# Kernel optimization log

Hardware: AMD Instinct MI355X
Metric: run time of the kernel (lower is better)

The kernel has to match this reference:

```python
import jax, jax.numpy as jnp
import numpy as np

N = 100_000      # nodes
E = 1_250_000    # edges (avg degree ~12.5)
D_IN, D_H, D_OUT = 64, 64, 64


def setup_inputs() -> dict:
    key = jax.random.key(0)
    ks = jax.random.split(key, 7)
    x = jax.random.normal(ks[0], (N, D_IN), dtype=jnp.float32)
    edge_index = jax.random.randint(ks[1], (2, E), 0, N, dtype=jnp.int32)
    edge_weight = jax.random.uniform(ks[2], (E,), dtype=jnp.float32)
    # GCNConv linear weights: PyG lin stores [out, in], applied as x @ W.T; bias added after aggregation.
    W1 = jax.random.normal(ks[3], (D_H, D_IN), dtype=jnp.float32) * (1.0 / np.sqrt(D_IN))
    b1 = jax.random.normal(ks[4], (D_H,), dtype=jnp.float32) * 0.01
    W2 = jax.random.normal(ks[5], (D_OUT, D_H), dtype=jnp.float32) * (1.0 / np.sqrt(D_H))
    b2 = jax.random.normal(ks[6], (D_OUT,), dtype=jnp.float32) * 0.01
    return {"x": x, "edge_index": edge_index, "edge_weight": edge_weight,
            "W1": W1, "b1": b1, "W2": W2, "b2": b2}


def _gcn_conv(x, src, dst, w, W, b, n_nodes):
    # PyG GCNConv: add self-loops (weight 1), symmetric normalization, linear, scatter-add, +bias.
    deg = jax.ops.segment_sum(w, dst, num_segments=n_nodes) + 1.0  # +1 from self-loop
    dis = jnp.where(deg > 0, jax.lax.rsqrt(deg), 0.0)              # deg^{-1/2}
    coef = dis[src] * w * dis[dst]                                 # per-edge norm, [E]
    h = x @ W.T                                                    # [N, out]
    agg = jax.ops.segment_sum(h[src] * coef[:, None], dst, num_segments=n_nodes)
    agg = agg + h * (dis * dis)[:, None]                           # self-loop: dis_i * 1 * dis_i
    return agg + b


def reference(x, edge_index, edge_weight, W1, b1, W2, b2):
    n = x.shape[0]
    src, dst = edge_index[0], edge_index[1]
    h = _gcn_conv(x, src, dst, edge_weight, W1, b1, n)
    h = jax.nn.relu(h)
    # dropout p=0.0 -> identity
    return _gcn_conv(h, src, dst, edge_weight, W2, b2, n)
```

## Files before the change

### kernel.cpp

```cpp
#include <hip/hip_runtime.h>


typedef unsigned int u32;
typedef unsigned short u16;

#define NBKT 256
#define LSH 9
#define BNODES 512
#define CAP 8192
#define SRCBITS 17
#define SRCMASK ((1u << SRCBITS) - 1u)

__device__ inline u16 f2bf(float f) {
  u32 u = __float_as_uint(f);
  u32 r = u + 0x7FFFu + ((u >> 16) & 1u);
  return (u16)(r >> 16);
}
__device__ inline float bf_lo(u32 p) { return __uint_as_float(p << 16); }
__device__ inline float bf_hi(u32 p) { return __uint_as_float(p & 0xFFFF0000u); }

__device__ inline u32 blockscan256_excl(u32 val, u32* wsum) {
  int lane = threadIdx.x & 63, wv = threadIdx.x >> 6;
  u32 inc = val;
  #pragma unroll
  for (int d = 1; d < 64; d <<= 1) {
    u32 t = __shfl_up(inc, d);
    if (lane >= d) inc += t;
  }
  if (lane == 63) wsum[wv] = inc;
  __syncthreads();
  u32 off = 0;
  #pragma unroll
  for (int i = 0; i < 4; ++i) if (i < wv) off += wsum[i];
  return off + inc - val;
}

__global__ void k_bin(const int* __restrict__ ei, u32* __restrict__ bucket_cnt,
                      u32* __restrict__ blockbase, int E, int chunk) {
  __shared__ u32 hist[NBKT];
  if (threadIdx.x < NBKT) hist[threadIdx.x] = 0u;
  __syncthreads();
  int e0 = blockIdx.x * chunk;
  int e1 = min(E, e0 + chunk);
  for (int e = e0 + (threadIdx.x << 1); e < e1; e += 512) {
    if (e + 1 < e1) {
      int2 dd = *(const int2*)(ei + E + e);
      atomicAdd(&hist[dd.x >> LSH], 1u);
      atomicAdd(&hist[dd.y >> LSH], 1u);
    } else {
      atomicAdd(&hist[ei[E + e] >> LSH], 1u);
    }
  }
  __syncthreads();
  if (threadIdx.x < NBKT)
    blockbase[threadIdx.x * 256 + blockIdx.x] =
        atomicAdd(&bucket_cnt[threadIdx.x], hist[threadIdx.x]);
}

__global__ __launch_bounds__(256, 4) void k_scatter_gemm(
    const int* __restrict__ ei, const float* __restrict__ w,
    const u32* __restrict__ blockbase,
    uint2* __restrict__ bucketed,
    const float* __restrict__ X, const float* __restrict__ W,
    u16* __restrict__ H, int N, int E, int chunk) {
  __shared__ float Wt[64 * 65];
  __shared__ float Xs[16 * 64];
  __shared__ u32 base[NBKT];
  int tid = threadIdx.x;
  if ((int)blockIdx.x < 256) {
    if (tid < NBKT)
      base[tid] = (u32)tid * CAP + blockbase[tid * 256 + blockIdx.x];
    __syncthreads();
    int e0 = blockIdx.x * chunk, e1 = min(E, e0 + chunk);
    for (int e = e0 + (tid << 1); e < e1; e += 512) {
      if (e + 1 < e1) {
        int2 ss = *(const int2*)(ei + e);
        int2 dd = *(const int2*)(ei + E + e);
        float2 wv = *(const float2*)(w + e);
        u32 p0 = atomicAdd(&base[dd.x >> LSH], 1u);
        u32 p1 = atomicAdd(&base[dd.y >> LSH], 1u);
        bucketed[p0] = make_uint2((u32)ss.x | ((u32)(dd.x & (BNODES - 1)) << SRCBITS),
                                  __float_as_uint(wv.x));
        bucketed[p1] = make_uint2((u32)ss.y | ((u32)(dd.y & (BNODES - 1)) << SRCBITS),
                                  __float_as_uint(wv.y));
      } else {
        int s = ei[e], d = ei[E + e];
        u32 pos = atomicAdd(&base[d >> LSH], 1u);
        bucketed[pos] = make_uint2((u32)s | ((u32)(d & (BNODES - 1)) << SRCBITS),
                                   __float_as_uint(w[e]));
      }
    }
    return;
  }
  int row0 = ((int)blockIdx.x - 256) * 16;
  if (row0 >= N) return;
  for (int i = tid; i < 4096; i += 256) Wt[(i & 63) * 65 + (i >> 6)] = W[i];
  {
    const float4* xsrc = (const float4*)(X + (size_t)row0 * 64);
    if (row0 + 16 <= N) {
      ((float4*)Xs)[tid] = xsrc[tid];
    } else {
      int r = tid >> 4;
      ((float4*)Xs)[tid] = (row0 + r < N) ? xsrc[tid]
                                          : make_float4(0.f, 0.f, 0.f, 0.f);
    }
  }
  __syncthreads();
  int lane = tid & 63, wv4 = tid >> 6;
  int rbase = wv4 * 4;
  float a0 = 0.f, a1 = 0.f, a2 = 0.f, a3 = 0.f;
  #pragma unroll 4
  for (int k4 = 0; k4 < 16; ++k4) {
    int k = k4 << 2;
    float w0 = Wt[k * 65 + lane], w1 = Wt[(k + 1) * 65 + lane];
    float w2 = Wt[(k + 2) * 65 + lane], w3 = Wt[(k + 3) * 65 + lane];
    float4 xa = *(const float4*)&Xs[(rbase + 0) * 64 + k];
    float4 xb = *(const float4*)&Xs[(rbase + 1) * 64 + k];
    float4 xc = *(const float4*)&Xs[(rbase + 2) * 64 + k];
    float4 xd = *(const float4*)&Xs[(rbase + 3) * 64 + k];
    a0 = fmaf(xa.x, w0, fmaf(xa.y, w1, fmaf(xa.z, w2, fmaf(xa.w, w3, a0))));
    a1 = fmaf(xb.x, w0, fmaf(xb.y, w1, fmaf(xb.z, w2, fmaf(xb.w, w3, a1))));
    a2 = fmaf(xc.x, w0, fmaf(xc.y, w1, fmaf(xc.z, w2, fmaf(xc.w, w3, a2))));
    a3 = fmaf(xd.x, w0, fmaf(xd.y, w1, fmaf(xd.z, w2, fmaf(xd.w, w3, a3))));
  }
  int row = row0 + rbase;
  if (row + 3 < N) {
    H[(size_t)row * 64 + lane]       = f2bf(a0);
    H[(size_t)(row + 1) * 64 + lane] = f2bf(a1);
    H[(size_t)(row + 2) * 64 + lane] = f2bf(a2);
    H[(size_t)(row + 3) * 64 + lane] = f2bf(a3);
  } else {
    if (row < N)     H[(size_t)row * 64 + lane]       = f2bf(a0);
    if (row + 1 < N) H[(size_t)(row + 1) * 64 + lane] = f2bf(a1);
    if (row + 2 < N) H[(size_t)(row + 2) * 64 + lane] = f2bf(a2);
    if (row + 3 < N) H[(size_t)(row + 3) * 64 + lane] = f2bf(a3);
  }
}

__global__ void k_statsfill(const uint2* __restrict__ bucketed,
                            const u32* __restrict__ bucket_cnt,
                            float* __restrict__ dis, int4* __restrict__ info,
                            int2* __restrict__ csr, u16* __restrict__ H, int N) {
  __shared__ u32 hist[BNODES];
  __shared__ u32 cur[BNODES];
  __shared__ float disl[BNODES];
  __shared__ u32 wsum[4];
  int b = blockIdx.x, tid = threadIdx.x;
  for (int i = tid; i < BNODES; i += 256) hist[i] = 0u;
  __syncthreads();
  u32 s0 = (u32)b * CAP, s1 = s0 + bucket_cnt[b];
  for (u32 p = s0 + tid; p < s1; p += 256) {
    uint2 ed = bucketed[p];
    u32 local = ed.x >> SRCBITS;
    u32 wfix = (u32)(__uint_as_float(ed.y) * 262144.0f);
    atomicAdd(&hist[local], (1u << 24) | wfix);
  }
  __syncthreads();
  u32 h0 = hist[2 * tid], h1 = hist[2 * tid + 1];
  u32 c0 = h0 >> 24, c1 = h1 >> 24;
  u32 excl = blockscan256_excl(c0 + c1, wsum);
  float d0 = rsqrtf(1.0f + (float)(h0 & 0xFFFFFFu) * (1.0f / 262144.0f));
  float d1 = rsqrtf(1.0f + (float)(h1 & 0xFFFFFFu) * (1.0f / 262144.0f));
  cur[2 * tid] = excl;
  cur[2 * tid + 1] = excl + c0;
  disl[2 * tid] = d0;
  disl[2 * tid + 1] = d1;
  int n0 = b * BNODES + 2 * tid;
  if (n0 < N) {
    dis[n0] = d0;
    info[n0] = make_int4((int)(s0 + excl), (int)c0, __float_as_int(d0), 0);
  }
  if (n0 + 1 < N) {
    dis[n0 + 1] = d1;
    info[n0 + 1] = make_int4((int)(s0 + excl + c0), (int)c1, __float_as_int(d1), 0);
  }
  __syncthreads();
  for (u32 p = s0 + tid; p < s1; p += 256) {
    uint2 ed = bucketed[p];
    u32 local = ed.x >> SRCBITS;
    u32 pos = atomicAdd(&cur[local], 1u);
    csr[s0 + pos] = make_int2((int)(ed.x & SRCMASK), (int)ed.y);
  }
  uint2* Hv = (uint2*)H;
  for (int i = tid; i < BNODES * 16; i += 256) {
    int row = i >> 4;
    int node = b * BNODES + row;
    if (node >= N) break;
    float dv = disl[row];
    size_t idx = (size_t)node * 16 + (i & 15);
    uint2 v = Hv[idx];
    u32 lo = (u32)f2bf(bf_lo(v.x) * dv) | ((u32)f2bf(bf_hi(v.x) * dv) << 16);
    u32 hi = (u32)f2bf(bf_lo(v.y) * dv) | ((u32)f2bf(bf_hi(v.y) * dv) << 16);
    Hv[idx] = make_uint2(lo, hi);
  }
}

__global__ __launch_bounds__(256, 6) void k_agg_gemm(
    const u16* __restrict__ H, const int4* __restrict__ info,
    const int2* __restrict__ csr, const float* __restrict__ bias,
    const float* __restrict__ W2, const float* __restrict__ dis,
    u16* __restrict__ H2, int N) {
  __shared__ float Wt[64 * 65];
  __shared__ float Ys[16 * 64];
  int tid = threadIdx.x;
  for (int i = tid; i < 4096; i += 256) Wt[(i & 63) * 65 + (i >> 6)] = W2[i];
  int node = blockIdx.x * 16 + (tid >> 4);
  int fid = (tid & 15) << 2;
  bool valid = node < N;
  int4 nfo = valid ? info[node] : make_int4(0, 0, 0, 0);
  int s0 = nfo.x, n = nfo.y;
  float d = __int_as_float(nfo.z);
  uint2 hs = valid ? *(const uint2*)(H + (size_t)node * 64 + fid)
                   : make_uint2(0u, 0u);
  float4 b4 = *(const float4*)(bias + fid);
  float4 acc = make_float4(0.f, 0.f, 0.f, 0.f);
  int nm1 = n - 1;
  for (int base = 0; base < n; base += 4) {
    int q1 = min(base + 1, nm1);
    int q2 = min(base + 2, nm1), q3 = min(base + 3, nm1);
    int2 c0 = csr[s0 + base];
    int2 c1 = csr[s0 + q1];
    int2 c2 = csr[s0 + q2];
    int2 c3 = csr[s0 + q3];
    uint2 h0 = *(const uint2*)(H + (size_t)c0.x * 64 + fid);
    uint2 h1 = *(const uint2*)(H + (size_t)c1.x * 64 + fid);
    uint2 h2 = *(const uint2*)(H + (size_t)c2.x * 64 + fid);
    uint2 h3 = *(const uint2*)(H + (size_t)c3.x * 64 + fid);
    float f0 = __int_as_float(c0.y);
    float f1 = (base + 1 < n) ? __int_as_float(c1.y) : 0.f;
    float f2 = (base + 2 < n) ? __int_as_float(c2.y) : 0.f;
    float f3 = (base + 3 < n) ? __int_as_float(c3.y) : 0.f;
    acc.x = fmaf(bf_lo(h0.x), f0, acc.x); acc.y = fmaf(bf_hi(h0.x), f0, acc.y);
    acc.z = fmaf(bf_lo(h0.y), f0, acc.z); acc.w = fmaf(bf_hi(h0.y), f0, acc.w);
    acc.x = fmaf(bf_lo(h1.x), f1, acc.x); acc.y = fmaf(bf_hi(h1.x), f1, acc.y);
    acc.z = fmaf(bf_lo(h1.y), f1, acc.z); acc.w = fmaf(bf_hi(h1.y), f1, acc.w);
    acc.x = fmaf(bf_lo(h2.x), f2, acc.x); acc.y = fmaf(bf_hi(h2.x), f2, acc.y);
    acc.z = fmaf(bf_lo(h2.y), f2, acc.z); acc.w = fmaf(bf_hi(h2.y), f2, acc.w);
    acc.x = fmaf(bf_lo(h3.x), f3, acc.x); acc.y = fmaf(bf_hi(h3.x), f3, acc.y);
    acc.z = fmaf(bf_lo(h3.y), f3, acc.z); acc.w = fmaf(bf_hi(h3.y), f3, acc.w);
  }
  if (valid) {
    acc.x = fmaxf((acc.x + bf_lo(hs.x)) * d + b4.x, 0.f);
    acc.y = fmaxf((acc.y + bf_hi(hs.x)) * d + b4.y, 0.f);
    acc.z = fmaxf((acc.z + bf_lo(hs.y)) * d + b4.z, 0.f);
    acc.w = fmaxf((acc.w + bf_hi(hs.y)) * d + b4.w, 0.f);
  } else {
    acc = make_float4(0.f, 0.f, 0.f, 0.f);
  }
  *(float4*)&Ys[(tid >> 4) * 64 + fid] = acc;
  __syncthreads();
  int lane = tid & 63, wv = tid >> 6;
  int rbase = wv * 4;
  int row0 = blockIdx.x * 16;
  float a0 = 0.f, a1 = 0.f, a2 = 0.f, a3 = 0.f;
  #pragma unroll 4
  for (int k4 = 0; k4 < 16; ++k4) {
    int k = k4 << 2;
    float w0 = Wt[k * 65 + lane], w1 = Wt[(k + 1) * 65 + lane];
    float w2 = Wt[(k + 2) * 65 + lane], w3 = Wt[(k + 3) * 65 + lane];
    float4 xa = *(const float4*)&Ys[(rbase + 0) * 64 + k];
    float4 xb = *(const float4*)&Ys[(rbase + 1) * 64 + k];
    float4 xc = *(const float4*)&Ys[(rbase + 2) * 64 + k];
    float4 xd = *(const float4*)&Ys[(rbase + 3) * 64 + k];
    a0 = fmaf(xa.x, w0, fmaf(xa.y, w1, fmaf(xa.z, w2, fmaf(xa.w, w3, a0))));
    a1 = fmaf(xb.x, w0, fmaf(xb.y, w1, fmaf(xb.z, w2, fmaf(xb.w, w3, a1))));
    a2 = fmaf(xc.x, w0, fmaf(xc.y, w1, fmaf(xc.z, w2, fmaf(xc.w, w3, a2))));
    a3 = fmaf(xd.x, w0, fmaf(xd.y, w1, fmaf(xd.z, w2, fmaf(xd.w, w3, a3))));
  }
  int row = row0 + rbase;
  if (row + 3 < N) {
    float dv0 = dis[row], dv1 = dis[row + 1], dv2 = dis[row + 2], dv3 = dis[row + 3];
    H2[(size_t)row * 64 + lane]       = f2bf(a0 * dv0);
    H2[(size_t)(row + 1) * 64 + lane] = f2bf(a1 * dv1);
    H2[(size_t)(row + 2) * 64 + lane] = f2bf(a2 * dv2);
    H2[(size_t)(row + 3) * 64 + lane] = f2bf(a3 * dv3);
  } else {
    if (row < N)     H2[(size_t)row * 64 + lane]       = f2bf(a0 * dis[row]);
    if (row + 1 < N) H2[(size_t)(row + 1) * 64 + lane] = f2bf(a1 * dis[row + 1]);
    if (row + 2 < N) H2[(size_t)(row + 2) * 64 + lane] = f2bf(a2 * dis[row + 2]);
    if (row + 3 < N) H2[(size_t)(row + 3) * 64 + lane] = f2bf(a3 * dis[row + 3]);
  }
}

__global__ __launch_bounds__(256, 8) void k_aggregate2(
    const u16* __restrict__ H, const int4* __restrict__ info,
    const int2* __restrict__ csr, const float* __restrict__ bias,
    float* __restrict__ Y, int N) {
  int tid = threadIdx.x;
  int node = blockIdx.x * 16 + (tid >> 4);
  int fid = (tid & 15) << 2;
  bool valid = node < N;
  int4 nfo = valid ? info[node] : make_int4(0, 0, 0, 0);
  int s0 = nfo.x, n = nfo.y;
  float d = __int_as_float(nfo.z);
  uint2 hs = valid ? *(const uint2*)(H + (size_t)node * 64 + fid)
                   : make_uint2(0u, 0u);
  float4 b4 = *(const float4*)(bias + fid);
  float4 acc = make_float4(0.f, 0.f, 0.f, 0.f);
  int nm1 = n - 1;
  for (int base = 0; base < n; base += 4) {
    int q1 = min(base + 1, nm1);
    int q2 = min(base + 2, nm1), q3 = min(base + 3, nm1);
    int2 c0 = csr[s0 + base];
    int2 c1 = csr[s0 + q1];
    int2 c2 = csr[s0 + q2];
    int2 c3 = csr[s0 + q3];
    uint2 h0 = *(const uint2*)(H + (size_t)c0.x * 64 + fid);
    uint2 h1 = *(const uint2*)(H + (size_t)c1.x * 64 + fid);
    uint2 h2 = *(const uint2*)(H + (size_t)c2.x * 64 + fid);
    uint2 h3 = *(const uint2*)(H + (size_t)c3.x * 64 + fid);
    float f0 = __int_as_float(c0.y);
    float f1 = (base + 1 < n) ? __int_as_float(c1.y) : 0.f;
    float f2 = (base + 2 < n) ? __int_as_float(c2.y) : 0.f;
    float f3 = (base + 3 < n) ? __int_as_float(c3.y) : 0.f;
    acc.x = fmaf(bf_lo(h0.x), f0, acc.x); acc.y = fmaf(bf_hi(h0.x), f0, acc.y);
    acc.z = fmaf(bf_lo(h0.y), f0, acc.z); acc.w = fmaf(bf_hi(h0.y), f0, acc.w);
    acc.x = fmaf(bf_lo(h1.x), f1, acc.x); acc.y = fmaf(bf_hi(h1.x), f1, acc.y);
    acc.z = fmaf(bf_lo(h1.y), f1, acc.z); acc.w = fmaf(bf_hi(h1.y), f1, acc.w);
    acc.x = fmaf(bf_lo(h2.x), f2, acc.x); acc.y = fmaf(bf_hi(h2.x), f2, acc.y);
    acc.z = fmaf(bf_lo(h2.y), f2, acc.z); acc.w = fmaf(bf_hi(h2.y), f2, acc.w);
    acc.x = fmaf(bf_lo(h3.x), f3, acc.x); acc.y = fmaf(bf_hi(h3.x), f3, acc.y);
    acc.z = fmaf(bf_lo(h3.y), f3, acc.z); acc.w = fmaf(bf_hi(h3.y), f3, acc.w);
  }
  if (valid) {
    acc.x = (acc.x + bf_lo(hs.x)) * d + b4.x;
    acc.y = (acc.y + bf_hi(hs.x)) * d + b4.y;
    acc.z = (acc.z + bf_lo(hs.y)) * d + b4.z;
    acc.w = (acc.w + bf_hi(hs.y)) * d + b4.w;
    *(float4*)(Y + (size_t)node * 64 + fid) = acc;
  }
}

extern "C" void kernel_launch(void* const* d_in, const int* in_sizes, int n_in,
                              void* d_out, int out_size, void* d_ws, size_t ws_size,
                              hipStream_t stream) {
  const float* x  = (const float*)d_in[0];
  const int*   ei = (const int*)d_in[1];
  const float* w  = (const float*)d_in[2];
  const float* W1 = (const float*)d_in[3];
  const float* b1 = (const float*)d_in[4];
  const float* W2 = (const float*)d_in[5];
  const float* b2 = (const float*)d_in[6];
  const int N = in_sizes[0] / 64;
  const int E = in_sizes[2];

  char* ws = (char*)d_ws;
  size_t off = 0;
  auto alloc = [&](size_t bytes) -> char* {
    char* p = ws + off;
    off = (off + bytes + 255) & ~(size_t)255;
    return p;
  };
  u32*   bucket_cnt   = (u32*)  alloc((size_t)NBKT * 4);
  u32*   blockbase    = (u32*)  alloc((size_t)NBKT * 256 * 4);
  uint2* bucketed     = (uint2*)alloc((size_t)NBKT * CAP * 8);
  int2*  csr          = (int2*) alloc((size_t)NBKT * CAP * 8);
  float* dis          = (float*)alloc((size_t)N * 4);
  int4*  info         = (int4*) alloc((size_t)N * 16);
  u16*   h1           = (u16*)  alloc((size_t)N * 64 * 2);
  u16*   h2           = (u16*)  alloc((size_t)N * 64 * 2);

  const int chunk = ((E + 511) / 512) * 2;
  const int nbG = (N + 15) / 16;
  const int nbA = (N + 15) / 16;
  const int nbB = (N + BNODES - 1) >> LSH;

  hipMemsetAsync(bucket_cnt, 0, (size_t)NBKT * 4, stream);
  k_bin<<<256, 256, 0, stream>>>(ei, bucket_cnt, blockbase, E, chunk);
  k_scatter_gemm<<<256 + nbG, 256, 0, stream>>>(ei, w, blockbase, bucketed,
                                                x, W1, h1, N, E, chunk);
  k_statsfill<<<nbB, 256, 0, stream>>>(bucketed, bucket_cnt, dis, info, csr, h1, N);
  k_agg_gemm<<<nbA, 256, 0, stream>>>(h1, info, csr, b1, W2, dis, h2, N);
  k_aggregate2<<<nbA, 256, 0, stream>>>(h2, info, csr, b2, (float*)d_out, N);
}
```

Baseline: 237.3 us.

## Pad CSR rows to multiples of four and degree-sort nodes within buckets

Each node's CSR segment is padded to a multiple of four with zero-weight entries, so the aggregation loops read two aligned int4 pairs per step with no clamping or masking. k_statsfill also builds a per-bucket permutation that orders nodes by in-degree (capped at 63) using a 64-bin counting sort. The aggregation kernels then process nodes in that order, so the 16-thread groups in a wavefront see similar loop trip counts and diverge less. The cost is extra CSR storage (CAP raised to 9216), an indirection through perm, scattered output writes, and padded entries that still gather row 0 of H.

```diff
diff --git a/kernel.cpp b/kernel.cpp
--- a/kernel.cpp
+++ b/kernel.cpp
@@ -7,7 +7,7 @@
 #define NBKT 256
 #define LSH 9
 #define BNODES 512
-#define CAP 8192
+#define CAP 9216
 #define SRCBITS 17
 #define SRCMASK ((1u << SRCBITS) - 1u)
 
@@ -140,13 +140,17 @@
 __global__ void k_statsfill(const uint2* __restrict__ bucketed,
                             const u32* __restrict__ bucket_cnt,
                             float* __restrict__ dis, int4* __restrict__ info,
-                            int2* __restrict__ csr, u16* __restrict__ H, int N) {
+                            int2* __restrict__ csr, u32* __restrict__ perm,
+                            u16* __restrict__ H, int N) {
   __shared__ u32 hist[BNODES];
   __shared__ u32 cur[BNODES];
   __shared__ float disl[BNODES];
   __shared__ u32 wsum[4];
+  __shared__ u32 dbin[64];
+  __shared__ u32 drank[64];
   int b = blockIdx.x, tid = threadIdx.x;
   for (int i = tid; i < BNODES; i += 256) hist[i] = 0u;
+  if (tid < 64) dbin[tid] = 0u;
   __syncthreads();
   u32 s0 = (u32)b * CAP, s1 = s0 + bucket_cnt[b];
   for (u32 p = s0 + tid; p < s1; p += 256) {
@@ -158,23 +162,41 @@
   __syncthreads();
   u32 h0 = hist[2 * tid], h1 = hist[2 * tid + 1];
   u32 c0 = h0 >> 24, c1 = h1 >> 24;
-  u32 excl = blockscan256_excl(c0 + c1, wsum);
+  u32 p0 = (c0 + 3u) & ~3u, p1 = (c1 + 3u) & ~3u;
+  u32 excl = blockscan256_excl(p0 + p1, wsum);
   float d0 = rsqrtf(1.0f + (float)(h0 & 0xFFFFFFu) * (1.0f / 262144.0f));
   float d1 = rsqrtf(1.0f + (float)(h1 & 0xFFFFFFu) * (1.0f / 262144.0f));
   cur[2 * tid] = excl;
-  cur[2 * tid + 1] = excl + c0;
+  cur[2 * tid + 1] = excl + p0;
   disl[2 * tid] = d0;
   disl[2 * tid + 1] = d1;
   int n0 = b * BNODES + 2 * tid;
-  if (n0 < N) {
+  bool v0 = n0 < N, v1 = n0 + 1 < N;
+  if (v0) {
     dis[n0] = d0;
-    info[n0] = make_int4((int)(s0 + excl), (int)c0, __float_as_int(d0), 0);
-  }
-  if (n0 + 1 < N) {
+    info[n0] = make_int4((int)(s0 + excl), (int)p0, __float_as_int(d0), 0);
+    atomicAdd(&dbin[min(c0, 63u)], 1u);
+  }
+  if (v1) {
     dis[n0 + 1] = d1;
-    info[n0 + 1] = make_int4((int)(s0 + excl + c0), (int)c1, __float_as_int(d1), 0);
-  }
-  __syncthreads();
+    info[n0 + 1] = make_int4((int)(s0 + excl + p0), (int)p1, __float_as_int(d1), 0);
+    atomicAdd(&dbin[min(c1, 63u)], 1u);
+  }
+  __syncthreads();
+  if (tid < 64) {
+    u32 v = dbin[tid], inc = v;
+    #pragma unroll
+    for (int d = 1; d < 64; d <<= 1) {
+      u32 t = __shfl_up(inc, d);
+      if (tid >= d) inc += t;
+    }
+    drank[tid] = inc - v;
+  }
+  __syncthreads();
+  if (v0) { u32 r = atomicAdd(&drank[min(c0, 63u)], 1u); perm[b * BNODES + r] = (u32)n0; }
+  if (v1) { u32 r = atomicAdd(&drank[min(c1, 63u)], 1u); perm[b * BNODES + r] = (u32)(n0 + 1); }
+  for (u32 j = c0; j < p0; ++j) csr[s0 + excl + j] = make_int2(0, 0);
+  for (u32 j = c1; j < p1; ++j) csr[s0 + excl + p0 + j] = make_int2(0, 0);
   for (u32 p = s0 + tid; p < s1; p += 256) {
     uint2 ed = bucketed[p];
     u32 local = ed.x >> SRCBITS;
@@ -197,39 +219,36 @@
 
 __global__ __launch_bounds__(256, 6) void k_agg_gemm(
     const u16* __restrict__ H, const int4* __restrict__ info,
-    const int2* __restrict__ csr, const float* __restrict__ bias,
-    const float* __restrict__ W2, const float* __restrict__ dis,
-    u16* __restrict__ H2, int N) {
+    const int2* __restrict__ csr, const u32* __restrict__ perm,
+    const float* __restrict__ bias, const float* __restrict__ W2,
+    const float* __restrict__ dis, u16* __restrict__ H2, int N) {
   __shared__ float Wt[64 * 65];
   __shared__ float Ys[16 * 64];
+  __shared__ u32 nids[16];
   int tid = threadIdx.x;
   for (int i = tid; i < 4096; i += 256) Wt[(i & 63) * 65 + (i >> 6)] = W2[i];
-  int node = blockIdx.x * 16 + (tid >> 4);
+  int slot = blockIdx.x * 16 + (tid >> 4);
   int fid = (tid & 15) << 2;
-  bool valid = node < N;
-  int4 nfo = valid ? info[node] : make_int4(0, 0, 0, 0);
+  bool valid = slot < N;
+  int nid = valid ? (int)perm[slot] : 0;
+  int4 nfo = valid ? info[nid] : make_int4(0, 0, 0, 0);
   int s0 = nfo.x, n = nfo.y;
   float d = __int_as_float(nfo.z);
-  uint2 hs = valid ? *(const uint2*)(H + (size_t)node * 64 + fid)
+  uint2 hs = valid ? *(const uint2*)(H + (size_t)nid * 64 + fid)
                    : make_uint2(0u, 0u);
   float4 b4 = *(const float4*)(bias + fid);
+  if ((tid & 15) == 0) nids[tid >> 4] = valid ? (u32)nid : 0xFFFFFFFFu;
   float4 acc = make_float4(0.f, 0.f, 0.f, 0.f);
-  int nm1 = n - 1;
+  const int4* c4 = (const int4*)(csr + s0);
   for (int base = 0; base < n; base += 4) {
-    int q1 = min(base + 1, nm1);
-    int q2 = min(base + 2, nm1), q3 = min(base + 3, nm1);
-    int2 c0 = csr[s0 + base];
-    int2 c1 = csr[s0 + q1];
-    int2 c2 = csr[s0 + q2];
-    int2 c3 = csr[s0 + q3];
-    uint2 h0 = *(const uint2*)(H + (size_t)c0.x * 64 + fid);
-    uint2 h1 = *(const uint2*)(H + (size_t)c1.x * 64 + fid);
-    uint2 h2 = *(const uint2*)(H + (size_t)c2.x * 64 + fid);
-    uint2 h3 = *(const uint2*)(H + (size_t)c3.x * 64 + fid);
-    float f0 = __int_as_float(c0.y);
-    float f1 = (base + 1 < n) ? __int_as_float(c1.y) : 0.f;
-    float f2 = (base + 2 < n) ? __int_as_float(c2.y) : 0.f;
-    float f3 = (base + 3 < n) ? __int_as_float(c3.y) : 0.f;
+    int4 ca = c4[base >> 1];
+    int4 cb = c4[(base >> 1) + 1];
+    uint2 h0 = *(const uint2*)(H + (size_t)ca.x * 64 + fid);
+    uint2 h1 = *(const uint2*)(H + (size_t)ca.z * 64 + fid);
+    uint2 h2 = *(const uint2*)(H + (size_t)cb.x * 64 + fid);
+    uint2 h3 = *(const uint2*)(H + (size_t)cb.z * 64 + fid);
+    float f0 = __int_as_float(ca.y), f1 = __int_as_float(ca.w);
+    float f2 = __int_as_float(cb.y), f3 = __int_as_float(cb.w);
     acc.x = fmaf(bf_lo(h0.x), f0, acc.x); acc.y = fmaf(bf_hi(h0.x), f0, acc.y);
     acc.z = fmaf(bf_lo(h0.y), f0, acc.z); acc.w = fmaf(bf_hi(h0.y), f0, acc.w);
     acc.x = fmaf(bf_lo(h1.x), f1, acc.x); acc.y = fmaf(bf_hi(h1.x), f1, acc.y);
@@ -251,7 +270,6 @@
   __syncthreads();
   int lane = tid & 63, wv = tid >> 6;
   int rbase = wv * 4;
-  int row0 = blockIdx.x * 16;
   float a0 = 0.f, a1 = 0.f, a2 = 0.f, a3 = 0.f;
   #pragma unroll 4
   for (int k4 = 0; k4 < 16; ++k4) {
@@ -267,52 +285,40 @@
     a2 = fmaf(xc.x, w0, fmaf(xc.y, w1, fmaf(xc.z, w2, fmaf(xc.w, w3, a2))));
     a3 = fmaf(xd.x, w0, fmaf(xd.y, w1, fmaf(xd.z, w2, fmaf(xd.w, w3, a3))));
   }
-  int row = row0 + rbase;
-  if (row + 3 < N) {
-    float dv0 = dis[row], dv1 = dis[row + 1], dv2 = dis[row + 2], dv3 = dis[row + 3];
-    H2[(size_t)row * 64 + lane]       = f2bf(a0 * dv0);
-    H2[(size_t)(row + 1) * 64 + lane] = f2bf(a1 * dv1);
-    H2[(size_t)(row + 2) * 64 + lane] = f2bf(a2 * dv2);
-    H2[(size_t)(row + 3) * 64 + lane] = f2bf(a3 * dv3);
-  } else {
-    if (row < N)     H2[(size_t)row * 64 + lane]       = f2bf(a0 * dis[row]);
-    if (row + 1 < N) H2[(size_t)(row + 1) * 64 + lane] = f2bf(a1 * dis[row + 1]);
-    if (row + 2 < N) H2[(size_t)(row + 2) * 64 + lane] = f2bf(a2 * dis[row + 2]);
-    if (row + 3 < N) H2[(size_t)(row + 3) * 64 + lane] = f2bf(a3 * dis[row + 3]);
-  }
+  u32 nr0 = nids[rbase], nr1 = nids[rbase + 1];
+  u32 nr2 = nids[rbase + 2], nr3 = nids[rbase + 3];
+  if (nr0 != 0xFFFFFFFFu) H2[(size_t)nr0 * 64 + lane] = f2bf(a0 * dis[nr0]);
+  if (nr1 != 0xFFFFFFFFu) H2[(size_t)nr1 * 64 + lane] = f2bf(a1 * dis[nr1]);
+  if (nr2 != 0xFFFFFFFFu) H2[(size_t)nr2 * 64 + lane] = f2bf(a2 * dis[nr2]);
+  if (nr3 != 0xFFFFFFFFu) H2[(size_t)nr3 * 64 + lane] = f2bf(a3 * dis[nr3]);
 }
 
 __global__ __launch_bounds__(256, 8) void k_aggregate2(
     const u16* __restrict__ H, const int4* __restrict__ info,
-    const int2* __restrict__ csr, const float* __restrict__ bias,
-    float* __restrict__ Y, int N) {
+    const int2* __restrict__ csr, const u32* __restrict__ perm,
+    const float* __restrict__ bias, float* __restrict__ Y, int N) {
   int tid = threadIdx.x;
-  int node = blockIdx.x * 16 + (tid >> 4);
+  int slot = blockIdx.x * 16 + (tid >> 4);
   int fid = (tid & 15) << 2;
-  bool valid = node < N;
-  int4 nfo = valid ? info[node] : make_int4(0, 0, 0, 0);
+  bool valid = slot < N;
+  int nid = valid ? (int)perm[slot] : 0;
+  int4 nfo = valid ? info[nid] : make_int4(0, 0, 0, 0);
   int s0 = nfo.x, n = nfo.y;
   float d = __int_as_float(nfo.z);
-  uint2 hs = valid ? *(const uint2*)(H + (size_t)node * 64 + fid)
+  uint2 hs = valid ? *(const uint2*)(H + (size_t)nid * 64 + fid)
                    : make_uint2(0u, 0u);
   float4 b4 = *(const float4*)(bias + fid);
   float4 acc = make_float4(0.f, 0.f, 0.f, 0.f);
-  int nm1 = n - 1;
+  const int4* c4 = (const int4*)(csr + s0);
   for (int base = 0; base < n; base += 4) {
-    int q1 = min(base + 1, nm1);
-    int q2 = min(base + 2, nm1), q3 = min(base + 3, nm1);
-    int2 c0 = csr[s0 + base];
-    int2 c1 = csr[s0 + q1];
-    int2 c2 = csr[s0 + q2];
-    int2 c3 = csr[s0 + q3];
-    uint2 h0 = *(const uint2*)(H + (size_t)c0.x * 64 + fid);
-    uint2 h1 = *(const uint2*)(H + (size_t)c1.x * 64 + fid);
-    uint2 h2 = *(const uint2*)(H + (size_t)c2.x * 64 + fid);
-    uint2 h3 = *(const uint2*)(H + (size_t)c3.x * 64 + fid);
-    float f0 = __int_as_float(c0.y);
-    float f1 = (base + 1 < n) ? __int_as_float(c1.y) : 0.f;
-    float f2 = (base + 2 < n) ? __int_as_float(c2.y) : 0.f;
-    float f3 = (base + 3 < n) ? __int_as_float(c3.y) : 0.f;
+    int4 ca = c4[base >> 1];
+    int4 cb = c4[(base >> 1) + 1];
+    uint2 h0 = *(const uint2*)(H + (size_t)ca.x * 64 + fid);
+    uint2 h1 = *(const uint2*)(H + (size_t)ca.z * 64 + fid);
+    uint2 h2 = *(const uint2*)(H + (size_t)cb.x * 64 + fid);
+    uint2 h3 = *(const uint2*)(H + (size_t)cb.z * 64 + fid);
+    float f0 = __int_as_float(ca.y), f1 = __int_as_float(ca.w);
+    float f2 = __int_as_float(cb.y), f3 = __int_as_float(cb.w);
     acc.x = fmaf(bf_lo(h0.x), f0, acc.x); acc.y = fmaf(bf_hi(h0.x), f0, acc.y);
     acc.z = fmaf(bf_lo(h0.y), f0, acc.z); acc.w = fmaf(bf_hi(h0.y), f0, acc.w);
     acc.x = fmaf(bf_lo(h1.x), f1, acc.x); acc.y = fmaf(bf_hi(h1.x), f1, acc.y);
@@ -327,7 +333,7 @@
     acc.y = (acc.y + bf_hi(hs.x)) * d + b4.y;
     acc.z = (acc.z + bf_lo(hs.y)) * d + b4.z;
     acc.w = (acc.w + bf_hi(hs.y)) * d + b4.w;
-    *(float4*)(Y + (size_t)node * 64 + fid) = acc;
+    *(float4*)(Y + (size_t)nid * 64 + fid) = acc;
   }
 }
 
@@ -357,6 +363,7 @@
   int2*  csr          = (int2*) alloc((size_t)NBKT * CAP * 8);
   float* dis          = (float*)alloc((size_t)N * 4);
   int4*  info         = (int4*) alloc((size_t)N * 16);
+  u32*   perm         = (u32*)  alloc((size_t)NBKT * BNODES * 4);
   u16*   h1           = (u16*)  alloc((size_t)N * 64 * 2);
   u16*   h2           = (u16*)  alloc((size_t)N * 64 * 2);
 
@@ -369,7 +376,8 @@
   k_bin<<<256, 256, 0, stream>>>(ei, bucket_cnt, blockbase, E, chunk);
   k_scatter_gemm<<<256 + nbG, 256, 0, stream>>>(ei, w, blockbase, bucketed,
                                                 x, W1, h1, N, E, chunk);
-  k_statsfill<<<nbB, 256, 0, stream>>>(bucketed, bucket_cnt, dis, info, csr, h1, N);
-  k_agg_gemm<<<nbA, 256, 0, stream>>>(h1, info, csr, b1, W2, dis, h2, N);
-  k_aggregate2<<<nbA, 256, 0, stream>>>(h2, info, csr, b2, (float*)d_out, N);
-}
+  k_statsfill<<<nbB, 256, 0, stream>>>(bucketed, bucket_cnt, dis, info, csr,
+                                       perm, h1, N);
+  k_agg_gemm<<<nbA, 256, 0, stream>>>(h1, info, csr, perm, b1, W2, dis, h2, N);
+  k_aggregate2<<<nbA, 256, 0, stream>>>(h2, info, csr, perm, b2, (float*)d_out, N);
+}
```

Result: slower. 249.5 us (+5.1%).
